# Performance work log

Measured on AMD Instinct MI355X. Metric: run time of the kernel, lower is better.

Reference implementation:

```python
import jax, jax.numpy as jnp
import numpy as np

B, S, H = 2, 2048, 1024
NH, HD = 16, 64  # num heads, head dim


def setup_inputs() -> dict:
    key = jax.random.key(0)
    ks = jax.random.split(key, 8)
    scale = 0.02
    return {
        "hidden_states": jax.random.normal(ks[0], (B, S, H), dtype=jnp.float32),
        "attention_mask": jnp.zeros((B, 1, 1, S), dtype=jnp.float32),
        "Wq": jax.random.normal(ks[1], (H, H), dtype=jnp.float32) * scale,
        "bq": jnp.zeros((H,), dtype=jnp.float32),
        "Wk": jax.random.normal(ks[2], (H, H), dtype=jnp.float32) * scale,
        "bk": jnp.zeros((H,), dtype=jnp.float32),
        "Wv": jax.random.normal(ks[3], (H, H), dtype=jnp.float32) * scale,
        "bv": jnp.zeros((H,), dtype=jnp.float32),
    }


def _split_heads(x):
    # [B,S,H] -> [B,NH,S,HD]
    b, s, _ = x.shape
    return x.reshape(b, s, NH, HD).transpose(0, 2, 1, 3)


def reference(hidden_states, attention_mask, Wq, bq, Wk, bk, Wv, bv):
    q = _split_heads(hidden_states @ Wq.T + bq)
    k = _split_heads(hidden_states @ Wk.T + bk)
    v = _split_heads(hidden_states @ Wv.T + bv)
    # scores: [B,NH,S,S]
    scores = jnp.einsum("bhqd,bhkd->bhqk", q, k) / jnp.sqrt(jnp.float32(HD))
    scores = scores + attention_mask
    att = jax.nn.softmax(scores, axis=-1)  # dropout is identity in eval
    ctx = jnp.einsum("bhqk,bhkd->bhqd", att, v)
    # [B,NH,S,HD] -> [B,S,H]
    return ctx.transpose(0, 2, 1, 3).reshape(hidden_states.shape[0], hidden_states.shape[1], NH * HD)
```

## Files before the change

kernel.cpp:

```cpp
#include <hip/hip_runtime.h>
#include <stdint.h>

#define BB 2
#define SS 2048
#define HH 1024
#define NH 16
#define HD 64

#define LOG2E 1.4426950408889634f
#define QSCALE (0.125f * LOG2E)

typedef short bfrag  __attribute__((ext_vector_type(8)));
typedef short bfrag4 __attribute__((ext_vector_type(4)));
typedef float f32x4  __attribute__((ext_vector_type(4)));

__device__ __forceinline__ short f2bf(float f) {
    union { float f; uint32_t u; } v; v.f = f;
    uint32_t r = (v.u + 0x7fffu + ((v.u >> 16) & 1u)) >> 16;
    return (short)r;
}

__global__ __launch_bounds__(256) void cvt_all(
    const float* __restrict__ X,  const float* __restrict__ Wq,
    const float* __restrict__ Wk, const float* __restrict__ Wv,
    const float* __restrict__ mask,
    short* __restrict__ Xb, short* __restrict__ Wcat,
    float* __restrict__ maskl)
{
    int i = blockIdx.x * 256 + threadIdx.x;
    if (i >= 1835008) {
        int off = i - 1835008;
        float4 f = ((const float4*)mask)[off];
        f.x *= LOG2E; f.y *= LOG2E; f.z *= LOG2E; f.w *= LOG2E;
        ((float4*)maskl)[off] = f;
        return;
    }
    const float* src; short* dst; int off;
    if (i < 1048576)      { src = X;  dst = Xb;                 off = i; }
    else if (i < 1310720) { src = Wq; dst = Wcat;               off = i - 1048576; }
    else if (i < 1572864) { src = Wk; dst = Wcat + 1048576;     off = i - 1310720; }
    else                  { src = Wv; dst = Wcat + 2097152;     off = i - 1572864; }
    float4 f = ((const float4*)src)[off];
    short4 s;
    s.x = f2bf(f.x); s.y = f2bf(f.y); s.z = f2bf(f.z); s.w = f2bf(f.w);
    ((short4*)dst)[off] = s;
}

__device__ __forceinline__ void gload_lds16(const void* g, void* lds) {
    __builtin_amdgcn_global_load_lds(
        (__attribute__((address_space(1))) void*)(uintptr_t)g,
        (__attribute__((address_space(3))) void*)(uintptr_t)lds,
        16, 0, 0);
}

__global__ __launch_bounds__(256, 2) void qkv_gemm(
    const short* __restrict__ X, const short* __restrict__ Wcat,
    const float* __restrict__ bq, const float* __restrict__ bk, const float* __restrict__ bv,
    short* __restrict__ Qo, short* __restrict__ Ko, short* __restrict__ Vo)
{
    __shared__ __align__(16) short smem[17408];
    short* As = smem;
    short* Bs = smem + 8192;

    const int tid  = threadIdx.x;
    const int wave = tid >> 6, lane = tid & 63;
    const int quad = lane >> 4, l15 = lane & 15;
    const int mTile = blockIdx.y * 128;
    const int nTile = blockIdx.x * 128;
    const int z = nTile >> 10;
    const int nLocT = nTile & 1023;
    const float* bias = (z == 0) ? bq : (z == 1) ? bk : bv;

    f32x4 acc[4][4];
#pragma unroll
    for (int i = 0; i < 4; ++i)
#pragma unroll
        for (int j = 0; j < 4; ++j) acc[i][j] = (f32x4)0.0f;

    const int srow  = lane >> 3;
    const int c_lin = lane & 7;
    const int mBase = (wave >> 1) * 64;
    const int nBase = (wave & 1) * 64;

    for (int k0 = 0; k0 < 1024; k0 += 64) {
        __syncthreads();
#pragma unroll
        for (int i = 0; i < 4; ++i) {
            int row = i * 32 + wave * 8 + srow;
            int cg  = c_lin ^ (row & 7);
            gload_lds16(X + (size_t)(mTile + row) * 1024 + k0 + cg * 8,
                        (char*)As + i * 4096 + wave * 1024);
            gload_lds16(Wcat + (size_t)(nTile + row) * 1024 + k0 + cg * 8,
                        (char*)Bs + i * 4096 + wave * 1024);
        }
        __syncthreads();

#pragma unroll
        for (int kt = 0; kt < 2; ++kt) {
            bfrag af[4], bf[4];
#pragma unroll
            for (int t = 0; t < 4; ++t) {
                int arow = mBase + t * 16 + l15;
                int aslot = (kt * 4 + quad) ^ (arow & 7);
                af[t] = *(const bfrag*)((const char*)As + arow * 128 + aslot * 16);
                int brow = nBase + t * 16 + l15;
                int bslot = (kt * 4 + quad) ^ (brow & 7);
                bf[t] = *(const bfrag*)((const char*)Bs + brow * 128 + bslot * 16);
            }
#pragma unroll
            for (int mt = 0; mt < 4; ++mt)
#pragma unroll
                for (int ct = 0; ct < 4; ++ct)
                    acc[mt][ct] = __builtin_amdgcn_mfma_f32_16x16x32_bf16(
                        af[mt], bf[ct], acc[mt][ct], 0, 0, 0);
        }
    }

    __syncthreads();
    const int b = mTile >> 11, sBase = mTile & 2047;

    if (z == 2) {
#pragma unroll
        for (int mt = 0; mt < 4; ++mt)
#pragma unroll
            for (int ct = 0; ct < 4; ++ct)
#pragma unroll
                for (int r = 0; r < 4; ++r) {
                    int nl = nBase + ct * 16 + l15;
                    int sl = mBase + mt * 16 + quad * 4 + r;
                    smem[nl * 136 + sl] = f2bf(acc[mt][ct][r] + bias[nLocT + nl]);
                }
        __syncthreads();
#pragma unroll
        for (int p = 0; p < 8; ++p) {
            int nl = p * 16 + (tid >> 4);
            int c  = tid & 15;
            bfrag v8 = *(const bfrag*)(smem + nl * 136 + c * 8);
            int ng = nLocT + nl, hh = ng >> 6, d = ng & 63;
            *(bfrag*)(Vo + ((size_t)(b * 16 + hh) * 64 + d) * 2048 + sBase + c * 8) = v8;
        }
    } else {
        short* Out = (z == 0) ? Qo : Ko;
        float scale = (z == 0) ? QSCALE : 1.0f;
#pragma unroll
        for (int mt = 0; mt < 4; ++mt)
#pragma unroll
            for (int ct = 0; ct < 4; ++ct)
#pragma unroll
                for (int r = 0; r < 4; ++r) {
                    int ml = mBase + mt * 16 + quad * 4 + r;
                    int nl = nBase + ct * 16 + l15;
                    smem[ml * 136 + nl] = f2bf((acc[mt][ct][r] + bias[nLocT + nl]) * scale);
                }
        __syncthreads();
#pragma unroll
        for (int p = 0; p < 8; ++p) {
            int ml = p * 16 + (tid >> 4);
            int c  = tid & 15;
            bfrag v8 = *(const bfrag*)(smem + ml * 136 + c * 8);
            int s  = sBase + ml;
            int nl = nLocT + c * 8, hh = nl >> 6, d = nl & 63;
            *(bfrag*)(Out + (((size_t)(b * 16 + hh) << 11) + s) * 64 + d) = v8;
        }
    }
}

__global__ __launch_bounds__(256, 4) void attn_kernel(
    const short* __restrict__ Qb, const short* __restrict__ Kb, const short* __restrict__ Vb,
    const float* __restrict__ maskl, float* __restrict__ out)
{
    __shared__ __align__(16) char smem[32768];
    char* KtB = smem;
    char* VtB = smem + 16384;

    const int tid  = threadIdx.x;
    const int wave = tid >> 6, lane = tid & 63;
    const int quad = lane >> 4, l15 = lane & 15;
    const int bh = blockIdx.y, b = bh >> 4, h = bh & 15;
    const int qBase = blockIdx.x * 64 + wave * 16;

    int koff[4], voff[4];
#pragma unroll
    for (int i = 0; i < 4; ++i) {
        int ci = wave * 256 + i * 64 + lane;
        { int r = ci >> 3, c = ci & 7;  koff[i] = r * 128  + (c ^ (r & 7))  * 16; }
        { int r = ci >> 4, c = ci & 15; voff[i] = r * 4096 + (c ^ (r & 15)) * 16; }
    }
    const char* kSrc = (const char*)(Kb + (size_t)bh * SS * HD);
    const char* vSrc = (const char*)(Vb + (size_t)bh * HD * SS);
    const char* mSrc = (const char*)(maskl + b * SS) + quad * 16;

    const short* Qp = Qb + ((size_t)bh * SS + qBase) * HD;
    bfrag qf[2];
#pragma unroll
    for (int kt = 0; kt < 2; ++kt)
        qf[kt] = *(const bfrag*)(Qp + (size_t)l15 * HD + kt * 32 + quad * 8);

    int kAddr[2];
#pragma unroll
    for (int kt = 0; kt < 2; ++kt)
        kAddr[kt] = l15 * 128 + (((kt * 4 + quad) ^ (l15 & 7)) * 16);
    int vAddr[8];
#pragma unroll
    for (int ct = 0; ct < 8; ++ct)
        vAddr[ct] = 16384 + l15 * 256 + (((ct * 2 + (quad >> 1)) ^ l15) * 16) + (quad & 1) * 8;

    const f32x4 z4 = (f32x4)0.0f;
    const bfrag4 ones = {0x3F80, 0x3F80, 0x3F80, 0x3F80};

    f32x4 oacc[4], ol = z4;
#pragma unroll
    for (int dt = 0; dt < 4; ++dt) oacc[dt] = z4;

    for (int j = 0; j < 16; ++j) {
        __syncthreads();
#pragma unroll
        for (int i = 0; i < 4; ++i)
            gload_lds16(kSrc + koff[i], KtB + (wave * 4 + i) * 1024);
#pragma unroll
        for (int i = 0; i < 4; ++i)
            gload_lds16(vSrc + voff[i], VtB + (wave * 4 + i) * 1024);
        kSrc += 16384; vSrc += 256;
        __syncthreads();

        f32x4 mvl[8];
#pragma unroll
        for (int ct = 0; ct < 8; ++ct)
            mvl[ct] = *(const f32x4*)(mSrc + ct * 64);
        mSrc += 512;

        f32x4 s[8];
#pragma unroll
        for (int ct = 0; ct < 8; ++ct) {
            bfrag kf0 = *(const bfrag*)(smem + kAddr[0] + ct * 2048);
            bfrag kf1 = *(const bfrag*)(smem + kAddr[1] + ct * 2048);
            s[ct] = __builtin_amdgcn_mfma_f32_16x16x32_bf16(kf0, qf[0], z4,    0, 0, 0);
            s[ct] = __builtin_amdgcn_mfma_f32_16x16x32_bf16(kf1, qf[1], s[ct], 0, 0, 0);
        }

        bfrag4 pf[8];
#pragma unroll
        for (int ct = 0; ct < 8; ++ct) {
            uint32_t a0 = __float_as_uint(exp2f(s[ct][0] + mvl[ct][0])) + 0x8000u;
            uint32_t a1 = __float_as_uint(exp2f(s[ct][1] + mvl[ct][1])) + 0x8000u;
            uint32_t a2 = __float_as_uint(exp2f(s[ct][2] + mvl[ct][2])) + 0x8000u;
            uint32_t a3 = __float_as_uint(exp2f(s[ct][3] + mvl[ct][3])) + 0x8000u;
            union { uint32_t u[2]; bfrag4 v; } cvt;
            cvt.u[0] = __builtin_amdgcn_perm(a1, a0, 0x07060302u);
            cvt.u[1] = __builtin_amdgcn_perm(a3, a2, 0x07060302u);
            pf[ct] = cvt.v;
        }

#pragma unroll
        for (int dt = 0; dt < 4; ++dt) {
#pragma unroll
            for (int ct = 0; ct < 8; ++ct) {
                bfrag4 vf = *(const bfrag4*)(smem + vAddr[ct] + dt * 4096);
                oacc[dt] = __builtin_amdgcn_mfma_f32_16x16x16bf16_1k(pf[ct], vf, oacc[dt], 0, 0, 0);
            }
        }
#pragma unroll
        for (int ct = 0; ct < 8; ++ct)
            ol = __builtin_amdgcn_mfma_f32_16x16x16bf16_1k(pf[ct], ones, ol, 0, 0, 0);
    }

#pragma unroll
    for (int r = 0; r < 4; ++r) {
        float linv = 1.0f / ol[r];
        int qrow = qBase + quad * 4 + r;
#pragma unroll
        for (int dt = 0; dt < 4; ++dt)
            out[((size_t)(b * SS + qrow)) * HH + h * 64 + dt * 16 + l15] =
                oacc[dt][r] * linv;
    }
}

extern "C" void kernel_launch(void* const* d_in, const int* in_sizes, int n_in,
                              void* d_out, int out_size, void* d_ws, size_t ws_size,
                              hipStream_t stream) {
    const float* hs   = (const float*)d_in[0];
    const float* mask = (const float*)d_in[1];
    const float* Wq   = (const float*)d_in[2];
    const float* bq   = (const float*)d_in[3];
    const float* Wk   = (const float*)d_in[4];
    const float* bk   = (const float*)d_in[5];
    const float* Wv   = (const float*)d_in[6];
    const float* bv   = (const float*)d_in[7];
    float* out = (float*)d_out;

    char* ws = (char*)d_ws;
    short* Xb    = (short*)(ws);
    short* Wcat  = (short*)(ws + (8ull  << 20));
    short* Qb    = (short*)(ws + (14ull << 20));
    short* Kb    = (short*)(ws + (22ull << 20));
    short* Vb    = (short*)(ws + (30ull << 20));
    float* maskl = (float*)(ws + (38ull << 20));

    cvt_all<<<7172, 256, 0, stream>>>(hs, Wq, Wk, Wv, mask, Xb, Wcat, maskl);

    qkv_gemm<<<dim3(24, 32), 256, 0, stream>>>(Xb, Wcat, bq, bk, bv, Qb, Kb, Vb);

    attn_kernel<<<dim3(SS / 64, BB * NH), 256, 0, stream>>>(Qb, Kb, Vb, maskl, out);
}
```

Before: 186.8 us.

## Replace direct global-to-LDS loads with register-prefetched staging in GEMM and attention

Both kernels drop the global_load_lds path. Each thread now prefetches the next K-slice (GEMM) or KV tile (attention) into registers while the current tile is being computed, then writes it to swizzled LDS after the barrier. The attention kernel halves its KV tile to 64 keys, which halves LDS to 16KB and doubles the iteration count. GEMM occupancy is raised to 3 blocks per SM. The aim is to hide global latency behind MFMA work, at the cost of more registers and extra LDS store instructions.

```diff
diff --git a/kernel.cpp b/kernel.cpp
--- a/kernel.cpp
+++ b/kernel.cpp
@@ -46,21 +46,12 @@
     ((short4*)dst)[off] = s;
 }
 
-__device__ __forceinline__ void gload_lds16(const void* g, void* lds) {
-    __builtin_amdgcn_global_load_lds(
-        (__attribute__((address_space(1))) void*)(uintptr_t)g,
-        (__attribute__((address_space(3))) void*)(uintptr_t)lds,
-        16, 0, 0);
-}
-
-__global__ __launch_bounds__(256, 2) void qkv_gemm(
+__global__ __launch_bounds__(256, 3) void qkv_gemm(
     const short* __restrict__ X, const short* __restrict__ Wcat,
     const float* __restrict__ bq, const float* __restrict__ bk, const float* __restrict__ bv,
     short* __restrict__ Qo, short* __restrict__ Ko, short* __restrict__ Vo)
 {
     __shared__ __align__(16) short smem[17408];
-    short* As = smem;
-    short* Bs = smem + 8192;
 
     const int tid  = threadIdx.x;
     const int wave = tid >> 6, lane = tid & 63;
@@ -77,23 +68,44 @@
 #pragma unroll
         for (int j = 0; j < 4; ++j) acc[i][j] = (f32x4)0.0f;
 
-    const int srow  = lane >> 3;
-    const int c_lin = lane & 7;
     const int mBase = (wave >> 1) * 64;
     const int nBase = (wave & 1) * 64;
 
+    int ls[4], ld[4];
+#pragma unroll
+    for (int i = 0; i < 4; ++i) {
+        int ci = tid + 256 * i;
+        int r = ci >> 3, c = ci & 7;
+        ls[i] = r * 2048 + c * 16;
+        ld[i] = r * 128 + ((c ^ (r & 7)) * 16);
+    }
+    const char* aPtr = (const char*)X + (size_t)mTile * 2048;
+    const char* bPtr = (const char*)Wcat + (size_t)nTile * 2048;
+
+    int4 areg[4], breg[4];
+#pragma unroll
+    for (int i = 0; i < 4; ++i) {
+        areg[i] = *(const int4*)(aPtr + ls[i]);
+        breg[i] = *(const int4*)(bPtr + ls[i]);
+    }
+    aPtr += 128; bPtr += 128;
+
     for (int k0 = 0; k0 < 1024; k0 += 64) {
         __syncthreads();
 #pragma unroll
         for (int i = 0; i < 4; ++i) {
-            int row = i * 32 + wave * 8 + srow;
-            int cg  = c_lin ^ (row & 7);
-            gload_lds16(X + (size_t)(mTile + row) * 1024 + k0 + cg * 8,
-                        (char*)As + i * 4096 + wave * 1024);
-            gload_lds16(Wcat + (size_t)(nTile + row) * 1024 + k0 + cg * 8,
-                        (char*)Bs + i * 4096 + wave * 1024);
-        }
-        __syncthreads();
+            *(int4*)((char*)smem + ld[i])          = areg[i];
+            *(int4*)((char*)smem + 16384 + ld[i])  = breg[i];
+        }
+        __syncthreads();
+        if (k0 < 960) {
+#pragma unroll
+            for (int i = 0; i < 4; ++i) {
+                areg[i] = *(const int4*)(aPtr + ls[i]);
+                breg[i] = *(const int4*)(bPtr + ls[i]);
+            }
+            aPtr += 128; bPtr += 128;
+        }
 
 #pragma unroll
         for (int kt = 0; kt < 2; ++kt) {
@@ -102,10 +114,10 @@
             for (int t = 0; t < 4; ++t) {
                 int arow = mBase + t * 16 + l15;
                 int aslot = (kt * 4 + quad) ^ (arow & 7);
-                af[t] = *(const bfrag*)((const char*)As + arow * 128 + aslot * 16);
+                af[t] = *(const bfrag*)((const char*)smem + arow * 128 + aslot * 16);
                 int brow = nBase + t * 16 + l15;
                 int bslot = (kt * 4 + quad) ^ (brow & 7);
-                bf[t] = *(const bfrag*)((const char*)Bs + brow * 128 + bslot * 16);
+                bf[t] = *(const bfrag*)((const char*)smem + 16384 + brow * 128 + bslot * 16);
             }
 #pragma unroll
             for (int mt = 0; mt < 4; ++mt)
@@ -169,9 +181,7 @@
     const short* __restrict__ Qb, const short* __restrict__ Kb, const short* __restrict__ Vb,
     const float* __restrict__ maskl, float* __restrict__ out)
 {
-    __shared__ __align__(16) char smem[32768];
-    char* KtB = smem;
-    char* VtB = smem + 16384;
+    __shared__ __align__(16) char smem[16384];
 
     const int tid  = threadIdx.x;
     const int wave = tid >> 6, lane = tid & 63;
@@ -179,15 +189,19 @@
     const int bh = blockIdx.y, b = bh >> 4, h = bh & 15;
     const int qBase = blockIdx.x * 64 + wave * 16;
 
-    int koff[4], voff[4];
-#pragma unroll
-    for (int i = 0; i < 4; ++i) {
-        int ci = wave * 256 + i * 64 + lane;
-        { int r = ci >> 3, c = ci & 7;  koff[i] = r * 128  + (c ^ (r & 7))  * 16; }
-        { int r = ci >> 4, c = ci & 15; voff[i] = r * 4096 + (c ^ (r & 15)) * 16; }
-    }
-    const char* kSrc = (const char*)(Kb + (size_t)bh * SS * HD);
-    const char* vSrc = (const char*)(Vb + (size_t)bh * HD * SS);
+    int kls[2], vls[2], kld[2], vld[2];
+#pragma unroll
+    for (int i = 0; i < 2; ++i) {
+        int ci = tid + 256 * i;
+        int r = ci >> 3, c = ci & 7;
+        int cs = (c ^ (r & 7)) * 16;
+        kls[i] = r * 128  + c * 16;
+        kld[i] = r * 128  + cs;
+        vls[i] = r * 4096 + c * 16;
+        vld[i] = 8192 + r * 128 + cs;
+    }
+    const char* kPtr = (const char*)(Kb + (size_t)bh * SS * HD);
+    const char* vPtr = (const char*)(Vb + (size_t)bh * HD * SS);
     const char* mSrc = (const char*)(maskl + b * SS) + quad * 16;
 
     const short* Qp = Qb + ((size_t)bh * SS + qBase) * HD;
@@ -200,10 +214,10 @@
 #pragma unroll
     for (int kt = 0; kt < 2; ++kt)
         kAddr[kt] = l15 * 128 + (((kt * 4 + quad) ^ (l15 & 7)) * 16);
-    int vAddr[8];
-#pragma unroll
-    for (int ct = 0; ct < 8; ++ct)
-        vAddr[ct] = 16384 + l15 * 256 + (((ct * 2 + (quad >> 1)) ^ l15) * 16) + (quad & 1) * 8;
+    int vAddr[4];
+#pragma unroll
+    for (int ct = 0; ct < 4; ++ct)
+        vAddr[ct] = 8192 + l15 * 128 + (((ct * 2 + (quad >> 1)) ^ (l15 & 7)) * 16) + (quad & 1) * 8;
 
     const f32x4 z4 = (f32x4)0.0f;
     const bfrag4 ones = {0x3F80, 0x3F80, 0x3F80, 0x3F80};
@@ -212,35 +226,49 @@
 #pragma unroll
     for (int dt = 0; dt < 4; ++dt) oacc[dt] = z4;
 
-    for (int j = 0; j < 16; ++j) {
-        __syncthreads();
-#pragma unroll
-        for (int i = 0; i < 4; ++i)
-            gload_lds16(kSrc + koff[i], KtB + (wave * 4 + i) * 1024);
-#pragma unroll
-        for (int i = 0; i < 4; ++i)
-            gload_lds16(vSrc + voff[i], VtB + (wave * 4 + i) * 1024);
-        kSrc += 16384; vSrc += 256;
-        __syncthreads();
-
-        f32x4 mvl[8];
-#pragma unroll
-        for (int ct = 0; ct < 8; ++ct)
+    int4 kreg[2], vreg[2];
+#pragma unroll
+    for (int i = 0; i < 2; ++i) {
+        kreg[i] = *(const int4*)(kPtr + kls[i]);
+        vreg[i] = *(const int4*)(vPtr + vls[i]);
+    }
+    kPtr += 8192; vPtr += 128;
+
+    for (int j = 0; j < 32; ++j) {
+        __syncthreads();
+#pragma unroll
+        for (int i = 0; i < 2; ++i) {
+            *(int4*)(smem + kld[i]) = kreg[i];
+            *(int4*)(smem + vld[i]) = vreg[i];
+        }
+        __syncthreads();
+        if (j < 31) {
+#pragma unroll
+            for (int i = 0; i < 2; ++i) {
+                kreg[i] = *(const int4*)(kPtr + kls[i]);
+                vreg[i] = *(const int4*)(vPtr + vls[i]);
+            }
+            kPtr += 8192; vPtr += 128;
+        }
+
+        f32x4 mvl[4];
+#pragma unroll
+        for (int ct = 0; ct < 4; ++ct)
             mvl[ct] = *(const f32x4*)(mSrc + ct * 64);
-        mSrc += 512;
-
-        f32x4 s[8];
-#pragma unroll
-        for (int ct = 0; ct < 8; ++ct) {
+        mSrc += 256;
+
+        f32x4 s[4];
+#pragma unroll
+        for (int ct = 0; ct < 4; ++ct) {
             bfrag kf0 = *(const bfrag*)(smem + kAddr[0] + ct * 2048);
             bfrag kf1 = *(const bfrag*)(smem + kAddr[1] + ct * 2048);
             s[ct] = __builtin_amdgcn_mfma_f32_16x16x32_bf16(kf0, qf[0], z4,    0, 0, 0);
             s[ct] = __builtin_amdgcn_mfma_f32_16x16x32_bf16(kf1, qf[1], s[ct], 0, 0, 0);
         }
 
-        bfrag4 pf[8];
-#pragma unroll
-        for (int ct = 0; ct < 8; ++ct) {
+        bfrag4 pf[4];
+#pragma unroll
+        for (int ct = 0; ct < 4; ++ct) {
             uint32_t a0 = __float_as_uint(exp2f(s[ct][0] + mvl[ct][0])) + 0x8000u;
             uint32_t a1 = __float_as_uint(exp2f(s[ct][1] + mvl[ct][1])) + 0x8000u;
             uint32_t a2 = __float_as_uint(exp2f(s[ct][2] + mvl[ct][2])) + 0x8000u;
@@ -254,13 +282,13 @@
 #pragma unroll
         for (int dt = 0; dt < 4; ++dt) {
 #pragma unroll
-            for (int ct = 0; ct < 8; ++ct) {
-                bfrag4 vf = *(const bfrag4*)(smem + vAddr[ct] + dt * 4096);
+            for (int ct = 0; ct < 4; ++ct) {
+                bfrag4 vf = *(const bfrag4*)(smem + vAddr[ct] + dt * 2048);
                 oacc[dt] = __builtin_amdgcn_mfma_f32_16x16x16bf16_1k(pf[ct], vf, oacc[dt], 0, 0, 0);
             }
         }
 #pragma unroll
-        for (int ct = 0; ct < 8; ++ct)
+        for (int ct = 0; ct < 4; ++ct)
             ol = __builtin_amdgcn_mfma_f32_16x16x16bf16_1k(pf[ct], ones, ol, 0, 0, 0);
     }
 
```

New measurement: 371.2 us. +98.8%, slower.
